# Optimization experiments

Hardware: AMD Instinct MI355X
Metric: run time of the kernel (lower is better)

## Reference

```python
import jax, jax.numpy as jnp
import numpy as np

D = 384      # n_embed_dims
H = 6        # n_heads
HS = D // H  # head_size = 64
T = 256      # block_size
B = 256
EPS = 1e-5


def setup_inputs() -> dict:
    key = jax.random.key(0)
    ks = jax.random.split(key, 12)
    s_in = 1.0 / np.sqrt(D)
    s_ff = 1.0 / np.sqrt(4 * D)
    return {
        "x": jax.random.normal(ks[0], (B, T, D), jnp.float32),
        # per-head QKV weights, stacked [H, D, HS] (Linear bias=False)
        "wq": jax.random.normal(ks[1], (H, D, HS), jnp.float32) * s_in,
        "wk": jax.random.normal(ks[2], (H, D, HS), jnp.float32) * s_in,
        "wv": jax.random.normal(ks[3], (H, D, HS), jnp.float32) * s_in,
        "w_proj": jax.random.normal(ks[4], (D, D), jnp.float32) * s_in,
        "b_proj": jax.random.normal(ks[5], (D,), jnp.float32) * s_in,
        "w1": jax.random.normal(ks[6], (D, 4 * D), jnp.float32) * s_in,
        "b1": jax.random.normal(ks[7], (4 * D,), jnp.float32) * s_in,
        "w2": jax.random.normal(ks[8], (4 * D, D), jnp.float32) * s_ff,
        "b2": jax.random.normal(ks[9], (D,), jnp.float32) * s_ff,
        "g1": jnp.ones((D,), jnp.float32),
        "be1": jnp.zeros((D,), jnp.float32),
        "g2": jnp.ones((D,), jnp.float32),
        "be2": jnp.zeros((D,), jnp.float32),
    }


def _layernorm(x, g, b):
    mu = jnp.mean(x, axis=-1, keepdims=True)
    var = jnp.mean(jnp.square(x - mu), axis=-1, keepdims=True)
    return (x - mu) * jax.lax.rsqrt(var + EPS) * g + b


def _attention(x, wq, wk, wv, w_proj, b_proj):
    # faithful quirk: scale = 1/sqrt(C) with C = full embed dim (384)
    scale = 1.0 / jnp.sqrt(jnp.asarray(D, x.dtype))
    q = jnp.einsum("btd,hde->bhte", x, wq)  # [B,H,T,HS]
    k = jnp.einsum("btd,hde->bhte", x, wk)
    v = jnp.einsum("btd,hde->bhte", x, wv)
    w = jnp.einsum("bhte,bhse->bhts", q, k) * scale  # [B,H,T,T], no mask
    w = jax.nn.softmax(w, axis=-1)
    out = jnp.einsum("bhts,bhse->bhte", w, v)  # [B,H,T,HS]
    # concat heads along feature dim (head order matches torch cat)
    out = out.transpose(0, 2, 1, 3).reshape(x.shape[0], x.shape[1], D)
    return out @ w_proj + b_proj


def reference(x, wq, wk, wv, w_proj, b_proj, w1, b1, w2, b2, g1, be1, g2, be2):
    x = x + _attention(_layernorm(x, g1, be1), wq, wk, wv, w_proj, b_proj)
    h = _layernorm(x, g2, be2)
    h = jax.nn.relu(h @ w1 + b1) @ w2 + b2  # dropout = eval-mode identity
    return x + h
```

## Files before the change

### kernel.cpp

```cpp
#include <hip/hip_runtime.h>
#include <stdint.h>

#define NTOK 65536
#define DE 384
#define QSTR 1280

typedef __bf16 bf16x8 __attribute__((ext_vector_type(8)));
typedef float  f32x4  __attribute__((ext_vector_type(4)));
typedef float  f32x16 __attribute__((ext_vector_type(16)));
typedef unsigned short u16x8 __attribute__((ext_vector_type(8)));

__device__ __forceinline__ unsigned short f2bf(float f) {
  union { float fl; unsigned u; } a; a.fl = f;
  unsigned r = a.u + 0x7fffu + ((a.u >> 16) & 1u);
  return (unsigned short)(r >> 16);
}
__device__ __forceinline__ float b2f(unsigned short s) {
  union { unsigned u; float f; } v; v.u = (unsigned)s << 16; return v.f;
}

__device__ __forceinline__ void gll16(const void* g, void* l) {
  __builtin_amdgcn_global_load_lds((const __attribute__((address_space(1))) void*)g,
                                   (__attribute__((address_space(3))) void*)l, 16, 0, 0);
}

__device__ __forceinline__ bf16x8 ds128(unsigned addr) {
  bf16x8 r;
  asm volatile("ds_read_b128 %0, %1" : "=v"(r) : "v"(addr));
  return r;
}

__global__ void pack_t(unsigned short* __restrict__ dst, const float* __restrict__ src,
                       int R, int C) {
  int t = blockIdx.x * 256 + threadIdx.x;
  if (t >= R * C) return;
  int r = t / C, c = t - r * C;
  dst[(size_t)c * R + r] = f2bf(src[t]);
}

__global__ void qkv_pack(const float* __restrict__ wq, const float* __restrict__ wk,
                         const float* __restrict__ wv, unsigned short* __restrict__ dst) {
  int t = blockIdx.x * 256 + threadIdx.x;
  if (t >= QSTR * 384) return;
  int n = t / 384, k = t - n * 384;
  unsigned short v = 0;
  if (n < 1152) {
    int which = n / 384, r = n - which * 384;
    const float* src = which == 0 ? wq : (which == 1 ? wk : wv);
    int h = r >> 6, e = r & 63;
    v = f2bf(src[h * 24576 + k * 64 + e]);
  }
  dst[t] = v;
}

__global__ __launch_bounds__(256) void ln_kernel(const float* __restrict__ x,
                                                 const float* __restrict__ g,
                                                 const float* __restrict__ be,
                                                 unsigned short* __restrict__ out) {
  int wave = threadIdx.x >> 6, lane = threadIdx.x & 63;
  size_t row = (size_t)blockIdx.x * 4 + wave;
  const float* xr = x + row * DE;
  int c0 = lane * 2;
  float2 v0 = *(const float2*)(xr + c0);
  float2 v1 = *(const float2*)(xr + 128 + c0);
  float2 v2 = *(const float2*)(xr + 256 + c0);
  float s  = v0.x + v0.y + v1.x + v1.y + v2.x + v2.y;
  float ss = v0.x*v0.x + v0.y*v0.y + v1.x*v1.x + v1.y*v1.y + v2.x*v2.x + v2.y*v2.y;
#pragma unroll
  for (int m = 1; m < 64; m <<= 1) { s += __shfl_xor(s, m); ss += __shfl_xor(ss, m); }
  float mu = s * (1.0f / 384.0f);
  float rstd = rsqrtf(ss * (1.0f / 384.0f) - mu * mu + 1e-5f);
  unsigned short* orow = out + row * DE;
  {
    float a0 = (v0.x - mu) * rstd * g[c0] + be[c0];
    float a1 = (v0.y - mu) * rstd * g[c0 + 1] + be[c0 + 1];
    *(unsigned*)(orow + c0) = (unsigned)f2bf(a0) | ((unsigned)f2bf(a1) << 16);
  }
  {
    int c = c0 + 128;
    float a0 = (v1.x - mu) * rstd * g[c] + be[c];
    float a1 = (v1.y - mu) * rstd * g[c + 1] + be[c + 1];
    *(unsigned*)(orow + c) = (unsigned)f2bf(a0) | ((unsigned)f2bf(a1) << 16);
  }
  {
    int c = c0 + 256;
    float a0 = (v2.x - mu) * rstd * g[c] + be[c];
    float a1 = (v2.y - mu) * rstd * g[c + 1] + be[c + 1];
    *(unsigned*)(orow + c) = (unsigned)f2bf(a0) | ((unsigned)f2bf(a1) << 16);
  }
}

template<int EPI>
__device__ __forceinline__
void gemm512_core(const unsigned short* __restrict__ A, const unsigned short* __restrict__ Bt,
                  int K, int Nst, int stride, int ntx,
                  const float* __restrict__ bias, const unsigned short* __restrict__ residb,
                  float* __restrict__ outf, unsigned short* __restrict__ outb) {
  __shared__ __align__(16) unsigned short As[2][512 * 32];
  __shared__ __align__(16) unsigned short Bs[2][192 * 32];
  const int tid = threadIdx.x;
  const int wave = tid >> 6, lane = tid & 63;

  const int nwg = gridDim.x;
  const int cpx = nwg >> 3;
  const int wg = (blockIdx.x & 7) * cpx + (blockIdx.x >> 3);
  const int bx = wg % ntx, by = wg / ntx;
  const int mBase = by << 9, nBase = bx * 192;
  const int wm = (wave >> 1) << 7;
  const int wn = (wave & 1) * 96;
  const int cr = lane & 31, hg = lane >> 5;

  const unsigned asb = (unsigned)(uintptr_t)&As[0][0];
  const unsigned bsb = (unsigned)(uintptr_t)&Bs[0][0];

  f32x16 acc[4][3];
#pragma unroll
  for (int i = 0; i < 4; ++i)
#pragma unroll
    for (int j = 0; j < 3; ++j)
#pragma unroll
      for (int r = 0; r < 16; ++r) acc[i][j][r] = 0.f;

  auto stageA = [&](int buf, int kt, int i) {
    int Lb = i * 8192 + wave * 1024;
    int L = Lb + lane * 16;
    int p = L >> 7;
    int sl = ((L >> 4) & 7) ^ (p & 7);
    int m = (p << 1) | (sl >> 2);
    int col = (sl & 3) << 3;
    gll16(A + (size_t)(mBase + m) * K + kt + col, (unsigned short*)As[buf] + (Lb >> 1));
  };
  auto stageB = [&](int buf, int kt, int i) {
    int Lb = i * 8192 + wave * 1024;
    if (Lb < 12288) {
      int L = Lb + lane * 16;
      int p = L >> 7;
      int sl = ((L >> 4) & 7) ^ (p & 7);
      int m = (p << 1) | (sl >> 2);
      int col = (sl & 3) << 3;
      gll16(Bt + (size_t)(nBase + m) * K + kt + col, (unsigned short*)Bs[buf] + (Lb >> 1));
    }
  };
  auto fraddr = [&](unsigned base, int row, int s) -> unsigned {
    return base + ((unsigned)(row >> 1) << 7) +
           ((unsigned)((s | ((row & 1) << 2)) ^ ((row >> 1) & 7)) << 4);
  };

  const int NK = K >> 5;
#pragma unroll
  for (int i = 0; i < 4; ++i) stageA(0, 0, i);
#pragma unroll
  for (int i = 0; i < 2; ++i) stageB(0, 0, i);

  for (int t = 0; t < NK; ++t) {
    const int cur = t & 1;
    if (t + 1 < NK) {
      const int kt = (t + 1) << 5;
#pragma unroll
      for (int i = 0; i < 4; ++i) stageA(cur ^ 1, kt, i);
#pragma unroll
      for (int i = 0; i < 2; ++i) stageB(cur ^ 1, kt, i);
      asm volatile("s_waitcnt vmcnt(5)" ::: "memory");
    } else {
      asm volatile("s_waitcnt vmcnt(0)" ::: "memory");
    }
    asm volatile("" ::: "memory");
    __builtin_amdgcn_s_barrier();
    asm volatile("" ::: "memory");

    const unsigned ab = asb + (cur ? 32768u : 0u);
    const unsigned bb = bsb + (cur ? 12288u : 0u);
#pragma unroll
    for (int ks = 0; ks < 2; ++ks) {
      const int s = ks * 2 + hg;
      bf16x8 bfr[3], af[4];
#pragma unroll
      for (int nt = 0; nt < 3; ++nt) bfr[nt] = ds128(fraddr(bb, wn + nt * 32 + cr, s));
#pragma unroll
      for (int mt = 0; mt < 4; ++mt) af[mt] = ds128(fraddr(ab, wm + mt * 32 + cr, s));
      asm volatile("s_waitcnt lgkmcnt(0)" ::: "memory");
      __builtin_amdgcn_sched_barrier(0);
      __builtin_amdgcn_s_setprio(1);
#pragma unroll
      for (int mt = 0; mt < 4; ++mt)
#pragma unroll
        for (int nt = 0; nt < 3; ++nt)
          acc[mt][nt] = __builtin_amdgcn_mfma_f32_32x32x16_bf16(af[mt], bfr[nt],
                                                                acc[mt][nt], 0, 0, 0);
      __builtin_amdgcn_s_setprio(0);
    }
    asm volatile("" ::: "memory");
    __builtin_amdgcn_s_barrier();
    asm volatile("" ::: "memory");
  }

#pragma unroll
  for (int mt = 0; mt < 4; ++mt) {
#pragma unroll
    for (int nt = 0; nt < 3; ++nt) {
      const int gn = nBase + wn + nt * 32 + cr;
      if (gn < Nst) {
#pragma unroll
        for (int r = 0; r < 16; ++r) {
          const int gm = mBase + wm + mt * 32 + (r & 3) + ((r >> 2) << 3) + (hg << 2);
          float val = acc[mt][nt][r];
          size_t idx = (size_t)gm * stride + gn;
          if (EPI == 0) {
            outb[idx] = f2bf(val);
          } else if (EPI == 2) {
            float rr = val + bias[gn];
            outb[idx] = f2bf(rr > 0.f ? rr : 0.f);
          } else {
            outf[idx] = val + bias[gn] + b2f(residb[idx]);
          }
        }
      }
    }
  }
}

__global__ __launch_bounds__(512, 2)
void gemm_qkv(const unsigned short* __restrict__ A, const unsigned short* __restrict__ Bt,
              int K, int Nst, int stride, int ntx, const float* __restrict__ bias,
              const unsigned short* __restrict__ residb, float* __restrict__ outf,
              unsigned short* __restrict__ outb) {
  gemm512_core<0>(A, Bt, K, Nst, stride, ntx, bias, residb, outf, outb);
}
__global__ __launch_bounds__(512, 2)
void gemm_mlp1(const unsigned short* __restrict__ A, const unsigned short* __restrict__ Bt,
               int K, int Nst, int stride, int ntx, const float* __restrict__ bias,
               const unsigned short* __restrict__ residb, float* __restrict__ outf,
               unsigned short* __restrict__ outb) {
  gemm512_core<2>(A, Bt, K, Nst, stride, ntx, bias, residb, outf, outb);
}
__global__ __launch_bounds__(512, 2)
void gemm_mlp2(const unsigned short* __restrict__ A, const unsigned short* __restrict__ Bt,
               int K, int Nst, int stride, int ntx, const float* __restrict__ bias,
               const unsigned short* __restrict__ residb, float* __restrict__ outf,
               unsigned short* __restrict__ outb) {
  gemm512_core<3>(A, Bt, K, Nst, stride, ntx, bias, residb, outf, outb);
}

__global__ __launch_bounds__(512, 1)
void gemm_projln(const unsigned short* __restrict__ A, const unsigned short* __restrict__ Bt,
                 int K, int stride, const float* __restrict__ bias,
                 const float* __restrict__ residf, const float* __restrict__ g2,
                 const float* __restrict__ be2, unsigned short* __restrict__ outb,
                 unsigned short* __restrict__ out2) {
  constexpr int BM = 128, BN = 384, WN = 4;
  constexpr int MT = 2, NT = 3;
  __shared__ __align__(16) unsigned short As[2][BM * 64];
  __shared__ __align__(16) unsigned short Bs[2][BN * 64];
  __shared__ float red[BM][4][2];
  const int tid = threadIdx.x;
  const int wave = tid >> 6, lane = tid & 63;

  const int nwg = gridDim.x;
  const int cpx = nwg >> 3;
  const int wg = (blockIdx.x & 7) * cpx + (blockIdx.x >> 3);
  const int mBase = wg * BM, nBase = 0;
  const int wni = wave % WN;
  const int wm = (wave / WN) * 64, wn = wni * 96;
  const int cr = lane & 31, hg = lane >> 5;

  const unsigned asb = (unsigned)(uintptr_t)&As[0][0];
  const unsigned bsb = (unsigned)(uintptr_t)&Bs[0][0];

  f32x16 acc[MT][NT];
#pragma unroll
  for (int i = 0; i < MT; ++i)
#pragma unroll
    for (int j = 0; j < NT; ++j)
#pragma unroll
      for (int r = 0; r < 16; ++r) acc[i][j][r] = 0.f;

  auto stage = [&](int buf, int kt) {
#pragma unroll
    for (int i = 0; i < 2; ++i) {
      int Lb = i * 8192 + wave * 1024;
      int L = Lb + lane * 16;
      int row = L >> 7;
      int col = ((((L >> 4) & 7) ^ (row & 7) ^ ((row >> 3) & 3)) << 3);
      gll16(A + (size_t)(mBase + row) * K + kt + col, (unsigned short*)As[buf] + (Lb >> 1));
    }
#pragma unroll
    for (int i = 0; i < 6; ++i) {
      int Lb = i * 8192 + wave * 1024;
      int L = Lb + lane * 16;
      int row = L >> 7;
      int col = ((((L >> 4) & 7) ^ (row & 7) ^ ((row >> 3) & 3)) << 3);
      gll16(Bt + (size_t)(nBase + row) * K + kt + col, (unsigned short*)Bs[buf] + (Lb >> 1));
    }
  };
  auto fraddr = [&](unsigned base, int row, int s) -> unsigned {
    return base + ((unsigned)(row << 7)) +
           ((unsigned)((s ^ (row & 7) ^ ((row >> 3) & 3)) & 7) << 4);
  };

  const int NK = K >> 6;
  stage(0, 0);
  for (int t = 0; t < NK; ++t) {
    const int cur = t & 1;
    if (t + 1 < NK) {
      stage(cur ^ 1, (t + 1) << 6);
      asm volatile("s_waitcnt vmcnt(8)" ::: "memory");
    } else {
      asm volatile("s_waitcnt vmcnt(0)" ::: "memory");
    }
    asm volatile("" ::: "memory");
    __builtin_amdgcn_s_barrier();
    asm volatile("" ::: "memory");

    const unsigned ab = asb + (cur ? (unsigned)(BM * 128) : 0u);
    const unsigned bb = bsb + (cur ? (unsigned)(BN * 128) : 0u);
#pragma unroll
    for (int ks = 0; ks < 4; ++ks) {
      const int s = ks * 2 + hg;
      bf16x8 bfr[NT], af[MT];
#pragma unroll
      for (int nt = 0; nt < NT; ++nt) bfr[nt] = ds128(fraddr(bb, wn + nt * 32 + cr, s));
#pragma unroll
      for (int mt = 0; mt < MT; ++mt) af[mt] = ds128(fraddr(ab, wm + mt * 32 + cr, s));
      asm volatile("s_waitcnt lgkmcnt(0)" ::: "memory");
      __builtin_amdgcn_sched_barrier(0);
      __builtin_amdgcn_s_setprio(1);
#pragma unroll
      for (int mt = 0; mt < MT; ++mt)
#pragma unroll
        for (int nt = 0; nt < NT; ++nt)
          acc[mt][nt] = __builtin_amdgcn_mfma_f32_32x32x16_bf16(af[mt], bfr[nt],
                                                                acc[mt][nt], 0, 0, 0);
      __builtin_amdgcn_s_setprio(0);
    }
    asm volatile("" ::: "memory");
    __builtin_amdgcn_s_barrier();
    asm volatile("" ::: "memory");
  }

#pragma unroll
  for (int mt = 0; mt < MT; ++mt)
#pragma unroll
    for (int nt = 0; nt < NT; ++nt) {
      const int gn = nBase + wn + nt * 32 + cr;
#pragma unroll
      for (int r = 0; r < 16; ++r) {
        const int gm = mBase + wm + mt * 32 + (r & 3) + ((r >> 2) << 3) + (hg << 2);
        size_t idx = (size_t)gm * stride + gn;
        acc[mt][nt][r] = acc[mt][nt][r] + bias[gn] + residf[idx];
      }
    }
#pragma unroll
  for (int mt = 0; mt < MT; ++mt)
#pragma unroll
    for (int r = 0; r < 16; ++r) {
      float s = 0.f, ss = 0.f;
#pragma unroll
      for (int nt = 0; nt < NT; ++nt) {
        float v = acc[mt][nt][r];
        s += v; ss += v * v;
      }
      s += __shfl_xor(s, 1);  ss += __shfl_xor(ss, 1);
      s += __shfl_xor(s, 2);  ss += __shfl_xor(ss, 2);
      s += __shfl_xor(s, 4);  ss += __shfl_xor(ss, 4);
      s += __shfl_xor(s, 8);  ss += __shfl_xor(ss, 8);
      s += __shfl_xor(s, 16); ss += __shfl_xor(ss, 16);
      if (cr == 0) {
        int row = wm + mt * 32 + (r & 3) + ((r >> 2) << 3) + (hg << 2);
        red[row][wni][0] = s;
        red[row][wni][1] = ss;
      }
    }
  __syncthreads();
#pragma unroll
  for (int mt = 0; mt < MT; ++mt)
#pragma unroll
    for (int r = 0; r < 16; ++r) {
      int row = wm + mt * 32 + (r & 3) + ((r >> 2) << 3) + (hg << 2);
      float s = red[row][0][0] + red[row][1][0] + red[row][2][0] + red[row][3][0];
      float ss = red[row][0][1] + red[row][1][1] + red[row][2][1] + red[row][3][1];
      float mu = s * (1.0f / 384.0f);
      float rstd = rsqrtf(ss * (1.0f / 384.0f) - mu * mu + 1e-5f);
      const int gm = mBase + row;
#pragma unroll
      for (int nt = 0; nt < NT; ++nt) {
        const int gn = nBase + wn + nt * 32 + cr;
        size_t idx = (size_t)gm * stride + gn;
        float x1v = acc[mt][nt][r];
        outb[idx] = f2bf(x1v);
        out2[idx] = f2bf((x1v - mu) * rstd * g2[gn] + be2[gn]);
      }
    }
}

__global__ __launch_bounds__(256)
void attn_kernel(const unsigned short* __restrict__ qkvn, unsigned short* __restrict__ o) {
  __shared__ unsigned short Vt[64 * 256];
  __shared__ unsigned short Pw[4][64 * 32];
  const int bh = blockIdx.x;
  const int b = bh / 6, h = bh - b * 6;
  const unsigned short* base = qkvn + (size_t)(b * 256) * QSTR;
  const unsigned short* qb = base + h * 64;
  const unsigned short* kbp = base + 384 + h * 64;
  const unsigned short* vbp = base + 768 + h * 64;
  const int wave = threadIdx.x >> 6, lane = threadIdx.x & 63;
  const int fr = lane & 15, fg = lane >> 4;
  const int fk = fg << 3;
  const int qrow0 = wave << 6;
  const float scale = 0.051031036307982884f;
  const f32x4 z = {0.f, 0.f, 0.f, 0.f};

  {
    const int s = threadIdx.x;
    u16x8 v8[8];
#pragma unroll
    for (int j = 0; j < 8; ++j)
      v8[j] = *(const u16x8*)(vbp + (size_t)s * QSTR + j * 8);
#pragma unroll
    for (int e = 0; e < 64; ++e)
      Vt[(e << 8) + (s ^ ((e & 7) << 3))] = v8[e >> 3][e & 7];
  }
  __syncthreads();

  bf16x8 qf[4][2];
#pragma unroll
  for (int rb = 0; rb < 4; ++rb)
#pragma unroll
    for (int ks = 0; ks < 2; ++ks)
      qf[rb][ks] = *(const bf16x8*)(qb + (size_t)(qrow0 + rb * 16 + fr) * QSTR + ks * 32 + fk);

  f32x4 oacc[4][4];
  float psum[4][4];
#pragma unroll
  for (int rb = 0; rb < 4; ++rb)
#pragma unroll
    for (int nb = 0; nb < 4; ++nb) oacc[rb][nb] = z;
#pragma unroll
  for (int rb = 0; rb < 4; ++rb)
#pragma unroll
    for (int i = 0; i < 4; ++i) psum[rb][i] = 0.f;

  for (int kb2 = 0; kb2 < 8; ++kb2) {
#pragma unroll
    for (int c2 = 0; c2 < 2; ++c2) {
      int cb = kb2 * 2 + c2;
      bf16x8 kf0 = *(const bf16x8*)(kbp + (size_t)(cb * 16 + fr) * QSTR + fk);
      bf16x8 kf1 = *(const bf16x8*)(kbp + (size_t)(cb * 16 + fr) * QSTR + 32 + fk);
#pragma unroll
      for (int rb = 0; rb < 4; ++rb) {
        f32x4 s = __builtin_amdgcn_mfma_f32_16x16x32_bf16(qf[rb][0], kf0, z, 0, 0, 0);
        s = __builtin_amdgcn_mfma_f32_16x16x32_bf16(qf[rb][1], kf1, s, 0, 0, 0);
#pragma unroll
        for (int i = 0; i < 4; ++i) {
          float p = __expf(fminf(scale * s[i], 60.f));
          psum[rb][i] += p;
          Pw[wave][(rb * 16 + (fg << 2) + i) * 32 + c2 * 16 + fr] = f2bf(p);
        }
      }
    }
    bf16x8 pa[4], vf[4];
#pragma unroll
    for (int rb = 0; rb < 4; ++rb) pa[rb] = *(const bf16x8*)(&Pw[wave][(rb * 16 + fr) * 32 + fk]);
#pragma unroll
    for (int nb = 0; nb < 4; ++nb) {
      int e = nb * 16 + fr;
      vf[nb] = *(const bf16x8*)(&Vt[(e << 8) + ((kb2 * 32 + fk) ^ ((e & 7) << 3))]);
    }
#pragma unroll
    for (int rb = 0; rb < 4; ++rb)
#pragma unroll
      for (int nb = 0; nb < 4; ++nb)
        oacc[rb][nb] = __builtin_amdgcn_mfma_f32_16x16x32_bf16(pa[rb], vf[nb], oacc[rb][nb], 0, 0, 0);
  }

  float rs[4][4];
#pragma unroll
  for (int rb = 0; rb < 4; ++rb)
#pragma unroll
    for (int i = 0; i < 4; ++i) {
      float v = psum[rb][i];
      v += __shfl_xor(v, 1);
      v += __shfl_xor(v, 2);
      v += __shfl_xor(v, 4);
      v += __shfl_xor(v, 8);
      rs[rb][i] = 1.0f / v;
    }

#pragma unroll
  for (int rb = 0; rb < 4; ++rb)
#pragma unroll
    for (int nb = 0; nb < 4; ++nb)
#pragma unroll
      for (int i = 0; i < 4; ++i) {
        int token = b * 256 + qrow0 + rb * 16 + (fg << 2) + i;
        int gcol = h * 64 + nb * 16 + fr;
        o[(size_t)token * DE + gcol] = f2bf(oacc[rb][nb][i] * rs[rb][i]);
      }
}

extern "C" void kernel_launch(void* const* d_in, const int* in_sizes, int n_in,
                              void* d_out, int out_size, void* d_ws, size_t ws_size,
                              hipStream_t stream) {
  const float* x     = (const float*)d_in[0];
  const float* wq    = (const float*)d_in[1];
  const float* wk    = (const float*)d_in[2];
  const float* wv    = (const float*)d_in[3];
  const float* wproj = (const float*)d_in[4];
  const float* bproj = (const float*)d_in[5];
  const float* w1    = (const float*)d_in[6];
  const float* b1    = (const float*)d_in[7];
  const float* w2    = (const float*)d_in[8];
  const float* b2    = (const float*)d_in[9];
  const float* g1    = (const float*)d_in[10];
  const float* be1   = (const float*)d_in[11];
  const float* g2    = (const float*)d_in[12];
  const float* be2   = (const float*)d_in[13];

  char* ws = (char*)d_ws;
  unsigned short* xln   = (unsigned short*)(ws + 0);
  unsigned short* x1b   = (unsigned short*)(ws + 0);
  unsigned short* qkvn  = (unsigned short*)(ws + 50331648);
  unsigned short* hbuf  = (unsigned short*)(ws + 100663296);
  unsigned short* act   = (unsigned short*)(ws + 150994944);
  unsigned short* attno = (unsigned short*)(ws + 218103808);
  unsigned short* wqkvt = (unsigned short*)(ws + 352321536);
  unsigned short* wprjt = (unsigned short*)(ws + 352321536 + 983040);
  unsigned short* w1t   = (unsigned short*)(ws + 352321536 + 983040 + 294912);
  unsigned short* w2t   = (unsigned short*)(ws + 352321536 + 983040 + 294912 + 1179648);

  qkv_pack<<<(QSTR * 384 + 255) / 256, 256, 0, stream>>>(wq, wk, wv, wqkvt);
  pack_t<<<(147456 + 255) / 256, 256, 0, stream>>>(wprjt, wproj, 384, 384);
  pack_t<<<(589824 + 255) / 256, 256, 0, stream>>>(w1t, w1, 384, 1536);
  pack_t<<<(589824 + 255) / 256, 256, 0, stream>>>(w2t, w2, 1536, 384);

  ln_kernel<<<NTOK / 4, 256, 0, stream>>>(x, g1, be1, xln);

  gemm_qkv<<<128 * 6, 512, 0, stream>>>(xln, wqkvt, 384, 1152, 1280, 6,
                                        nullptr, nullptr, nullptr, qkvn);

  attn_kernel<<<1536, 256, 0, stream>>>(qkvn, attno);

  gemm_projln<<<512, 512, 0, stream>>>(attno, wprjt, 384, 384,
                                       bproj, x, g2, be2, x1b, hbuf);

  gemm_mlp1<<<128 * 8, 512, 0, stream>>>(hbuf, w1t, 384, 1536, 1536, 8,
                                         b1, nullptr, nullptr, act);

  gemm_mlp2<<<128 * 2, 512, 0, stream>>>(act, w2t, 1536, 384, 384, 2,
                                         b2, x1b, (float*)d_out, nullptr);
}
```

Baseline: 519.0 us.

## Load GEMM B fragments directly from global into registers, retile all GEMMs

Every GEMM kernel (qkv, projln, mlp1, mlp2) now skips LDS staging for the weight operand. Each wave loads its B fragments with global_load_dwordx4 straight into registers, double-buffered across a K=64 step, while A is still staged through swizzled LDS. Tile shapes change to 256xBN with per-kernel warp layouts and launch bounds drop to one block per CU. This is meant to cut LDS traffic and footprint for the weights, which stay cache-resident. In exchange it needs many more VGPRs, lowers occupancy, and relies on hardcoded vmcnt waits that must match the issued load counts.

```diff
diff --git a/kernel.cpp b/kernel.cpp
--- a/kernel.cpp
+++ b/kernel.cpp
@@ -28,6 +28,17 @@
   bf16x8 r;
   asm volatile("ds_read_b128 %0, %1" : "=v"(r) : "v"(addr));
   return r;
+}
+
+__device__ __forceinline__ void ldg128(bf16x8& r, unsigned long long addr) {
+  asm volatile("global_load_dwordx4 %0, %1, off" : "=&v"(r) : "v"(addr));
+}
+
+template<int N> __device__ __forceinline__ void vmw() {
+  if constexpr (N == 0)       asm volatile("s_waitcnt vmcnt(0)" ::: "memory");
+  else if constexpr (N == 12) asm volatile("s_waitcnt vmcnt(12)" ::: "memory");
+  else if constexpr (N == 14) asm volatile("s_waitcnt vmcnt(14)" ::: "memory");
+  else                        asm volatile("s_waitcnt vmcnt(16)" ::: "memory");
 }
 
 __global__ void pack_t(unsigned short* __restrict__ dst, const float* __restrict__ src,
@@ -90,14 +101,17 @@
   }
 }
 
-template<int EPI>
+template<int EPI, int BM, int BN, int WM, int WN>
 __device__ __forceinline__
-void gemm512_core(const unsigned short* __restrict__ A, const unsigned short* __restrict__ Bt,
-                  int K, int Nst, int stride, int ntx,
+void gemm_bd_core(const unsigned short* __restrict__ A, const unsigned short* __restrict__ Bt,
+                  int K, int stride, int ntx,
                   const float* __restrict__ bias, const unsigned short* __restrict__ residb,
                   float* __restrict__ outf, unsigned short* __restrict__ outb) {
-  __shared__ __align__(16) unsigned short As[2][512 * 32];
-  __shared__ __align__(16) unsigned short Bs[2][192 * 32];
+  constexpr int MT = (BM / WM) / 32, NT = (BN / WN) / 32;
+  constexpr int LA = BM / 64;
+  constexpr int NB = 4 * NT;
+  constexpr int L = LA + NB;
+  __shared__ __align__(16) unsigned short As[2][BM * 64];
   const int tid = threadIdx.x;
   const int wave = tid >> 6, lane = tid & 63;
 
@@ -105,140 +119,146 @@
   const int cpx = nwg >> 3;
   const int wg = (blockIdx.x & 7) * cpx + (blockIdx.x >> 3);
   const int bx = wg % ntx, by = wg / ntx;
-  const int mBase = by << 9, nBase = bx * 192;
-  const int wm = (wave >> 1) << 7;
-  const int wn = (wave & 1) * 96;
+  const int mBase = by * BM, nBase = bx * BN;
+  const int wm = (wave / WN) * (BM / WM), wn = (wave % WN) * (BN / WN);
   const int cr = lane & 31, hg = lane >> 5;
 
   const unsigned asb = (unsigned)(uintptr_t)&As[0][0];
-  const unsigned bsb = (unsigned)(uintptr_t)&Bs[0][0];
-
-  f32x16 acc[4][3];
-#pragma unroll
-  for (int i = 0; i < 4; ++i)
-#pragma unroll
-    for (int j = 0; j < 3; ++j)
+
+  f32x16 acc[MT][NT];
+#pragma unroll
+  for (int i = 0; i < MT; ++i)
+#pragma unroll
+    for (int j = 0; j < NT; ++j)
 #pragma unroll
       for (int r = 0; r < 16; ++r) acc[i][j][r] = 0.f;
 
-  auto stageA = [&](int buf, int kt, int i) {
-    int Lb = i * 8192 + wave * 1024;
-    int L = Lb + lane * 16;
-    int p = L >> 7;
-    int sl = ((L >> 4) & 7) ^ (p & 7);
-    int m = (p << 1) | (sl >> 2);
-    int col = (sl & 3) << 3;
-    gll16(A + (size_t)(mBase + m) * K + kt + col, (unsigned short*)As[buf] + (Lb >> 1));
-  };
-  auto stageB = [&](int buf, int kt, int i) {
-    int Lb = i * 8192 + wave * 1024;
-    if (Lb < 12288) {
-      int L = Lb + lane * 16;
-      int p = L >> 7;
-      int sl = ((L >> 4) & 7) ^ (p & 7);
-      int m = (p << 1) | (sl >> 2);
-      int col = (sl & 3) << 3;
-      gll16(Bt + (size_t)(nBase + m) * K + kt + col, (unsigned short*)Bs[buf] + (Lb >> 1));
-    }
+  unsigned long long bb0[NT];
+#pragma unroll
+  for (int nt = 0; nt < NT; ++nt)
+    bb0[nt] = (unsigned long long)(uintptr_t)(Bt + (size_t)(nBase + wn + nt * 32 + cr) * K + hg * 8);
+
+  auto stageA = [&](int buf, int t) {
+    const int kt = t << 6;
+#pragma unroll
+    for (int i = 0; i < LA; ++i) {
+      int Lb = i * 8192 + wave * 1024;
+      int Lx = Lb + lane * 16;
+      int row = Lx >> 7;
+      int col = ((((Lx >> 4) & 7) ^ (row & 7) ^ ((row >> 3) & 3)) << 3);
+      gll16(A + (size_t)(mBase + row) * K + kt + col, (unsigned short*)As[buf] + (Lb >> 1));
+    }
+  };
+  auto loadB = [&](bf16x8 (&br)[4][NT], int t) {
+#pragma unroll
+    for (int ks = 0; ks < 4; ++ks)
+#pragma unroll
+      for (int nt = 0; nt < NT; ++nt)
+        ldg128(br[ks][nt], bb0[nt] + (unsigned)(t * 128 + ks * 32));
   };
   auto fraddr = [&](unsigned base, int row, int s) -> unsigned {
-    return base + ((unsigned)(row >> 1) << 7) +
-           ((unsigned)((s | ((row & 1) << 2)) ^ ((row >> 1) & 7)) << 4);
-  };
-
-  const int NK = K >> 5;
-#pragma unroll
-  for (int i = 0; i < 4; ++i) stageA(0, 0, i);
-#pragma unroll
-  for (int i = 0; i < 2; ++i) stageB(0, 0, i);
-
-  for (int t = 0; t < NK; ++t) {
-    const int cur = t & 1;
-    if (t + 1 < NK) {
-      const int kt = (t + 1) << 5;
-#pragma unroll
-      for (int i = 0; i < 4; ++i) stageA(cur ^ 1, kt, i);
-#pragma unroll
-      for (int i = 0; i < 2; ++i) stageB(cur ^ 1, kt, i);
-      asm volatile("s_waitcnt vmcnt(5)" ::: "memory");
-    } else {
-      asm volatile("s_waitcnt vmcnt(0)" ::: "memory");
-    }
-    asm volatile("" ::: "memory");
-    __builtin_amdgcn_s_barrier();
-    asm volatile("" ::: "memory");
-
-    const unsigned ab = asb + (cur ? 32768u : 0u);
-    const unsigned bb = bsb + (cur ? 12288u : 0u);
-#pragma unroll
-    for (int ks = 0; ks < 2; ++ks) {
-      const int s = ks * 2 + hg;
-      bf16x8 bfr[3], af[4];
-#pragma unroll
-      for (int nt = 0; nt < 3; ++nt) bfr[nt] = ds128(fraddr(bb, wn + nt * 32 + cr, s));
-#pragma unroll
-      for (int mt = 0; mt < 4; ++mt) af[mt] = ds128(fraddr(ab, wm + mt * 32 + cr, s));
+    return base + ((unsigned)(row << 7)) +
+           ((unsigned)((s ^ (row & 7) ^ ((row >> 3) & 3)) & 7) << 4);
+  };
+  auto compute = [&](unsigned ab, bf16x8 (&br)[4][NT]) {
+#pragma unroll
+    for (int k2 = 0; k2 < 2; ++k2) {
+      bf16x8 af[2][MT];
+#pragma unroll
+      for (int kk = 0; kk < 2; ++kk)
+#pragma unroll
+        for (int mt = 0; mt < MT; ++mt)
+          af[kk][mt] = ds128(fraddr(ab, wm + mt * 32 + cr, (k2 * 2 + kk) * 2 + hg));
       asm volatile("s_waitcnt lgkmcnt(0)" ::: "memory");
       __builtin_amdgcn_sched_barrier(0);
       __builtin_amdgcn_s_setprio(1);
 #pragma unroll
-      for (int mt = 0; mt < 4; ++mt)
-#pragma unroll
-        for (int nt = 0; nt < 3; ++nt)
-          acc[mt][nt] = __builtin_amdgcn_mfma_f32_32x32x16_bf16(af[mt], bfr[nt],
-                                                                acc[mt][nt], 0, 0, 0);
+      for (int kk = 0; kk < 2; ++kk)
+#pragma unroll
+        for (int mt = 0; mt < MT; ++mt)
+#pragma unroll
+          for (int nt = 0; nt < NT; ++nt)
+            acc[mt][nt] = __builtin_amdgcn_mfma_f32_32x32x16_bf16(af[kk][mt], br[k2 * 2 + kk][nt],
+                                                                  acc[mt][nt], 0, 0, 0);
       __builtin_amdgcn_s_setprio(0);
     }
-    asm volatile("" ::: "memory");
-    __builtin_amdgcn_s_barrier();
-    asm volatile("" ::: "memory");
-  }
-
-#pragma unroll
-  for (int mt = 0; mt < 4; ++mt) {
-#pragma unroll
-    for (int nt = 0; nt < 3; ++nt) {
+  };
+
+  bf16x8 brA[4][NT], brB[4][NT];
+  const int NH = (K >> 6) >> 1;
+  stageA(0, 0);
+  loadB(brA, 0);
+  for (int tp = 0; tp < NH; ++tp) {
+    const int t0 = tp * 2;
+    stageA(1, t0 + 1);
+    loadB(brB, t0 + 1);
+    vmw<L>();
+    asm volatile("" ::: "memory");
+    __builtin_amdgcn_s_barrier();
+    asm volatile("" ::: "memory");
+    compute(asb, brA);
+    asm volatile("" ::: "memory");
+    __builtin_amdgcn_s_barrier();
+    asm volatile("" ::: "memory");
+    if (tp + 1 < NH) {
+      stageA(0, t0 + 2);
+      loadB(brA, t0 + 2);
+      vmw<L>();
+    } else {
+      vmw<0>();
+    }
+    asm volatile("" ::: "memory");
+    __builtin_amdgcn_s_barrier();
+    asm volatile("" ::: "memory");
+    compute(asb + (unsigned)(BM * 128), brB);
+    asm volatile("" ::: "memory");
+    __builtin_amdgcn_s_barrier();
+    asm volatile("" ::: "memory");
+  }
+
+#pragma unroll
+  for (int mt = 0; mt < MT; ++mt) {
+#pragma unroll
+    for (int nt = 0; nt < NT; ++nt) {
       const int gn = nBase + wn + nt * 32 + cr;
-      if (gn < Nst) {
-#pragma unroll
-        for (int r = 0; r < 16; ++r) {
-          const int gm = mBase + wm + mt * 32 + (r & 3) + ((r >> 2) << 3) + (hg << 2);
-          float val = acc[mt][nt][r];
-          size_t idx = (size_t)gm * stride + gn;
-          if (EPI == 0) {
-            outb[idx] = f2bf(val);
-          } else if (EPI == 2) {
-            float rr = val + bias[gn];
-            outb[idx] = f2bf(rr > 0.f ? rr : 0.f);
-          } else {
-            outf[idx] = val + bias[gn] + b2f(residb[idx]);
-          }
+#pragma unroll
+      for (int r = 0; r < 16; ++r) {
+        const int gm = mBase + wm + mt * 32 + (r & 3) + ((r >> 2) << 3) + (hg << 2);
+        float val = acc[mt][nt][r];
+        size_t idx = (size_t)gm * stride + gn;
+        if (EPI == 0) {
+          outb[idx] = f2bf(val);
+        } else if (EPI == 2) {
+          float rr = val + bias[gn];
+          outb[idx] = f2bf(rr > 0.f ? rr : 0.f);
+        } else {
+          outf[idx] = val + bias[gn] + b2f(residb[idx]);
         }
       }
     }
   }
 }
 
-__global__ __launch_bounds__(512, 2)
+__global__ __launch_bounds__(512, 1)
 void gemm_qkv(const unsigned short* __restrict__ A, const unsigned short* __restrict__ Bt,
-              int K, int Nst, int stride, int ntx, const float* __restrict__ bias,
+              int K, int stride, int ntx, const float* __restrict__ bias,
               const unsigned short* __restrict__ residb, float* __restrict__ outf,
               unsigned short* __restrict__ outb) {
-  gemm512_core<0>(A, Bt, K, Nst, stride, ntx, bias, residb, outf, outb);
-}
-__global__ __launch_bounds__(512, 2)
+  gemm_bd_core<0, 256, 192, 4, 2>(A, Bt, K, stride, ntx, bias, residb, outf, outb);
+}
+__global__ __launch_bounds__(512, 1)
 void gemm_mlp1(const unsigned short* __restrict__ A, const unsigned short* __restrict__ Bt,
-               int K, int Nst, int stride, int ntx, const float* __restrict__ bias,
+               int K, int stride, int ntx, const float* __restrict__ bias,
                const unsigned short* __restrict__ residb, float* __restrict__ outf,
                unsigned short* __restrict__ outb) {
-  gemm512_core<2>(A, Bt, K, Nst, stride, ntx, bias, residb, outf, outb);
-}
-__global__ __launch_bounds__(512, 2)
+  gemm_bd_core<2, 256, 256, 2, 4>(A, Bt, K, stride, ntx, bias, residb, outf, outb);
+}
+__global__ __launch_bounds__(512, 1)
 void gemm_mlp2(const unsigned short* __restrict__ A, const unsigned short* __restrict__ Bt,
-               int K, int Nst, int stride, int ntx, const float* __restrict__ bias,
+               int K, int stride, int ntx, const float* __restrict__ bias,
                const unsigned short* __restrict__ residb, float* __restrict__ outf,
                unsigned short* __restrict__ outb) {
-  gemm512_core<3>(A, Bt, K, Nst, stride, ntx, bias, residb, outf, outb);
+  gemm_bd_core<3, 256, 128, 4, 2>(A, Bt, K, stride, ntx, bias, residb, outf, outb);
 }
 
 __global__ __launch_bounds__(512, 1)
@@ -247,10 +267,10 @@
                  const float* __restrict__ residf, const float* __restrict__ g2,
                  const float* __restrict__ be2, unsigned short* __restrict__ outb,
                  unsigned short* __restrict__ out2) {
-  constexpr int BM = 128, BN = 384, WN = 4;
+  constexpr int BM = 128, WN = 4;
   constexpr int MT = 2, NT = 3;
+  constexpr int LA = 2, NB = 12, L = LA + NB;
   __shared__ __align__(16) unsigned short As[2][BM * 64];
-  __shared__ __align__(16) unsigned short Bs[2][BN * 64];
   __shared__ float red[BM][4][2];
   const int tid = threadIdx.x;
   const int wave = tid >> 6, lane = tid & 63;
@@ -258,13 +278,12 @@
   const int nwg = gridDim.x;
   const int cpx = nwg >> 3;
   const int wg = (blockIdx.x & 7) * cpx + (blockIdx.x >> 3);
-  const int mBase = wg * BM, nBase = 0;
+  const int mBase = wg * BM;
   const int wni = wave % WN;
   const int wm = (wave / WN) * 64, wn = wni * 96;
   const int cr = lane & 31, hg = lane >> 5;
 
   const unsigned asb = (unsigned)(uintptr_t)&As[0][0];
-  const unsigned bsb = (unsigned)(uintptr_t)&Bs[0][0];
 
   f32x16 acc[MT][NT];
 #pragma unroll
@@ -274,64 +293,84 @@
 #pragma unroll
       for (int r = 0; r < 16; ++r) acc[i][j][r] = 0.f;
 
-  auto stage = [&](int buf, int kt) {
-#pragma unroll
-    for (int i = 0; i < 2; ++i) {
+  unsigned long long bb0[NT];
+#pragma unroll
+  for (int nt = 0; nt < NT; ++nt)
+    bb0[nt] = (unsigned long long)(uintptr_t)(Bt + (size_t)(wn + nt * 32 + cr) * K + hg * 8);
+
+  auto stageA = [&](int buf, int t) {
+    const int kt = t << 6;
+#pragma unroll
+    for (int i = 0; i < LA; ++i) {
       int Lb = i * 8192 + wave * 1024;
-      int L = Lb + lane * 16;
-      int row = L >> 7;
-      int col = ((((L >> 4) & 7) ^ (row & 7) ^ ((row >> 3) & 3)) << 3);
+      int Lx = Lb + lane * 16;
+      int row = Lx >> 7;
+      int col = ((((Lx >> 4) & 7) ^ (row & 7) ^ ((row >> 3) & 3)) << 3);
       gll16(A + (size_t)(mBase + row) * K + kt + col, (unsigned short*)As[buf] + (Lb >> 1));
     }
-#pragma unroll
-    for (int i = 0; i < 6; ++i) {
-      int Lb = i * 8192 + wave * 1024;
-      int L = Lb + lane * 16;
-      int row = L >> 7;
-      int col = ((((L >> 4) & 7) ^ (row & 7) ^ ((row >> 3) & 3)) << 3);
-      gll16(Bt + (size_t)(nBase + row) * K + kt + col, (unsigned short*)Bs[buf] + (Lb >> 1));
-    }
+  };
+  auto loadB = [&](bf16x8 (&br)[4][NT], int t) {
+#pragma unroll
+    for (int ks = 0; ks < 4; ++ks)
+#pragma unroll
+      for (int nt = 0; nt < NT; ++nt)
+        ldg128(br[ks][nt], bb0[nt] + (unsigned)(t * 128 + ks * 32));
   };
   auto fraddr = [&](unsigned base, int row, int s) -> unsigned {
     return base + ((unsigned)(row << 7)) +
            ((unsigned)((s ^ (row & 7) ^ ((row >> 3) & 3)) & 7) << 4);
   };
-
-  const int NK = K >> 6;
-  stage(0, 0);
-  for (int t = 0; t < NK; ++t) {
-    const int cur = t & 1;
-    if (t + 1 < NK) {
-      stage(cur ^ 1, (t + 1) << 6);
-      asm volatile("s_waitcnt vmcnt(8)" ::: "memory");
-    } else {
-      asm volatile("s_waitcnt vmcnt(0)" ::: "memory");
-    }
-    asm volatile("" ::: "memory");
-    __builtin_amdgcn_s_barrier();
-    asm volatile("" ::: "memory");
-
-    const unsigned ab = asb + (cur ? (unsigned)(BM * 128) : 0u);
-    const unsigned bb = bsb + (cur ? (unsigned)(BN * 128) : 0u);
-#pragma unroll
-    for (int ks = 0; ks < 4; ++ks) {
-      const int s = ks * 2 + hg;
-      bf16x8 bfr[NT], af[MT];
-#pragma unroll
-      for (int nt = 0; nt < NT; ++nt) bfr[nt] = ds128(fraddr(bb, wn + nt * 32 + cr, s));
-#pragma unroll
-      for (int mt = 0; mt < MT; ++mt) af[mt] = ds128(fraddr(ab, wm + mt * 32 + cr, s));
+  auto compute = [&](unsigned ab, bf16x8 (&br)[4][NT]) {
+#pragma unroll
+    for (int k2 = 0; k2 < 2; ++k2) {
+      bf16x8 af[2][MT];
+#pragma unroll
+      for (int kk = 0; kk < 2; ++kk)
+#pragma unroll
+        for (int mt = 0; mt < MT; ++mt)
+          af[kk][mt] = ds128(fraddr(ab, wm + mt * 32 + cr, (k2 * 2 + kk) * 2 + hg));
       asm volatile("s_waitcnt lgkmcnt(0)" ::: "memory");
       __builtin_amdgcn_sched_barrier(0);
       __builtin_amdgcn_s_setprio(1);
 #pragma unroll
-      for (int mt = 0; mt < MT; ++mt)
-#pragma unroll
-        for (int nt = 0; nt < NT; ++nt)
-          acc[mt][nt] = __builtin_amdgcn_mfma_f32_32x32x16_bf16(af[mt], bfr[nt],
-                                                                acc[mt][nt], 0, 0, 0);
+      for (int kk = 0; kk < 2; ++kk)
+#pragma unroll
+        for (int mt = 0; mt < MT; ++mt)
+#pragma unroll
+          for (int nt = 0; nt < NT; ++nt)
+            acc[mt][nt] = __builtin_amdgcn_mfma_f32_32x32x16_bf16(af[kk][mt], br[k2 * 2 + kk][nt],
+                                                                  acc[mt][nt], 0, 0, 0);
       __builtin_amdgcn_s_setprio(0);
     }
+  };
+
+  bf16x8 brA[4][NT], brB[4][NT];
+  const int NH = (K >> 6) >> 1;
+  stageA(0, 0);
+  loadB(brA, 0);
+  for (int tp = 0; tp < NH; ++tp) {
+    const int t0 = tp * 2;
+    stageA(1, t0 + 1);
+    loadB(brB, t0 + 1);
+    vmw<L>();
+    asm volatile("" ::: "memory");
+    __builtin_amdgcn_s_barrier();
+    asm volatile("" ::: "memory");
+    compute(asb, brA);
+    asm volatile("" ::: "memory");
+    __builtin_amdgcn_s_barrier();
+    asm volatile("" ::: "memory");
+    if (tp + 1 < NH) {
+      stageA(0, t0 + 2);
+      loadB(brA, t0 + 2);
+      vmw<L>();
+    } else {
+      vmw<0>();
+    }
+    asm volatile("" ::: "memory");
+    __builtin_amdgcn_s_barrier();
+    asm volatile("" ::: "memory");
+    compute(asb + (unsigned)(BM * 128), brB);
     asm volatile("" ::: "memory");
     __builtin_amdgcn_s_barrier();
     asm volatile("" ::: "memory");
@@ -341,7 +380,7 @@
   for (int mt = 0; mt < MT; ++mt)
 #pragma unroll
     for (int nt = 0; nt < NT; ++nt) {
-      const int gn = nBase + wn + nt * 32 + cr;
+      const int gn = wn + nt * 32 + cr;
 #pragma unroll
       for (int r = 0; r < 16; ++r) {
         const int gm = mBase + wm + mt * 32 + (r & 3) + ((r >> 2) << 3) + (hg << 2);
@@ -383,7 +422,7 @@
       const int gm = mBase + row;
 #pragma unroll
       for (int nt = 0; nt < NT; ++nt) {
-        const int gn = nBase + wn + nt * 32 + cr;
+        const int gn = wn + nt * 32 + cr;
         size_t idx = (size_t)gm * stride + gn;
         float x1v = acc[mt][nt][r];
         outb[idx] = f2bf(x1v);
@@ -534,7 +573,7 @@
 
   ln_kernel<<<NTOK / 4, 256, 0, stream>>>(x, g1, be1, xln);
 
-  gemm_qkv<<<128 * 6, 512, 0, stream>>>(xln, wqkvt, 384, 1152, 1280, 6,
+  gemm_qkv<<<256 * 6, 512, 0, stream>>>(xln, wqkvt, 384, 1280, 6,
                                         nullptr, nullptr, nullptr, qkvn);
 
   attn_kernel<<<1536, 256, 0, stream>>>(qkvn, attno);
@@ -542,9 +581,9 @@
   gemm_projln<<<512, 512, 0, stream>>>(attno, wprjt, 384, 384,
                                        bproj, x, g2, be2, x1b, hbuf);
 
-  gemm_mlp1<<<128 * 8, 512, 0, stream>>>(hbuf, w1t, 384, 1536, 1536, 8,
+  gemm_mlp1<<<256 * 6, 512, 0, stream>>>(hbuf, w1t, 384, 1536, 6,
                                          b1, nullptr, nullptr, act);
 
-  gemm_mlp2<<<128 * 2, 512, 0, stream>>>(act, w2t, 1536, 384, 384, 2,
+  gemm_mlp2<<<256 * 3, 512, 0, stream>>>(act, w2t, 1536, 384, 3,
                                          b2, x1b, (float*)d_out, nullptr);
 }
```

Result: slower. 811.7 us (+56.4%).
